# Kernel tuning notes

Measured on AMD Instinct MI355X. Metric: run time of the kernel, lower is better.

The kernel has to match this reference:

```python
import jax, jax.numpy as jnp
import numpy as np

N = 100000
E = 1000000
F_NODE = 64
F_EDGE = 32
H = 128
C_NODE = 12
C_EDGE = 4


def _glorot(key, shape):
    fan_in, fan_out = shape[0], shape[1]
    s = (6.0 / (fan_in + fan_out)) ** 0.5
    return jax.random.uniform(key, shape, jnp.float32, -s, s)


def setup_inputs() -> dict:
    key = jax.random.key(0)
    ks = jax.random.split(key, 16)
    x = jax.random.normal(ks[0], (N, F_NODE), jnp.float32)
    edge_index = jax.random.randint(ks[1], (2, E), 0, N, jnp.int32)
    edge_attr = jax.random.normal(ks[2], (E, F_EDGE), jnp.float32)
    return {
        "x": x,
        "edge_index": edge_index,
        "edge_attr": edge_attr,
        "We": _glorot(ks[3], (F_NODE, H)), "be": jnp.zeros((H,), jnp.float32),
        "Wc1": _glorot(ks[4], (H, H)), "bc1": jnp.zeros((H,), jnp.float32),
        "Wc2": _glorot(ks[5], (H, H)), "bc2": jnp.zeros((H,), jnp.float32),
        "Wn1": _glorot(ks[6], (H, H // 2)), "bn1": jnp.zeros((H // 2,), jnp.float32),
        "Wn2": _glorot(ks[7], (H // 2, C_NODE)), "bn2": jnp.zeros((C_NODE,), jnp.float32),
        "Wedge1": _glorot(ks[8], (2 * H + F_EDGE, H)), "bedge1": jnp.zeros((H,), jnp.float32),
        "Wedge2": _glorot(ks[9], (H, C_EDGE)), "bedge2": jnp.zeros((C_EDGE,), jnp.float32),
    }


def _gcn_conv(x, W, b, src, tgt, n):
    # PyG GCNConv: add self-loops, symmetric deg normalization, scatter-add.
    xw = x @ W  # [N, H]
    loop = jnp.arange(n, dtype=src.dtype)
    s = jnp.concatenate([src, loop])
    t = jnp.concatenate([tgt, loop])
    deg = jax.ops.segment_sum(jnp.ones_like(t, jnp.float32), t, num_segments=n)
    dinv = jnp.where(deg > 0, jax.lax.rsqrt(jnp.maximum(deg, 1.0)), 0.0)
    norm = dinv[s] * dinv[t]  # [E+N]
    msg = xw[s] * norm[:, None]
    return jax.ops.segment_sum(msg, t, num_segments=n) + b


def reference(x, edge_index, edge_attr, We, be, Wc1, bc1, Wc2, bc2,
              Wn1, bn1, Wn2, bn2, Wedge1, bedge1, Wedge2, bedge2):
    n = x.shape[0]
    row, col = edge_index[0], edge_index[1]
    h = jax.nn.relu(x @ We + be)          # node_embed Linear+ReLU
    h = jax.nn.relu(h)                     # extra F.relu in forward
    h = jax.nn.relu(_gcn_conv(h, Wc1, bc1, row, col, n))
    h = jax.nn.relu(_gcn_conv(h, Wc2, bc2, row, col, n))
    node_logits = jax.nn.relu(h @ Wn1 + bn1) @ Wn2 + bn2
    e = jnp.concatenate([h[row], h[col], edge_attr], axis=-1)  # [E, 2H+Fe]
    edge_logits = jax.nn.relu(e @ Wedge1 + bedge1) @ Wedge2 + bedge2
    return (node_logits, edge_logits)
```

## Files before the change

kernel.cpp:

```cpp
#include <hip/hip_runtime.h>

#define N_NODES 100000
#define N_EDGES 1000000
#define NB_SCAN 391
#define EDGE_OUT_BASE 1200000

typedef __attribute__((ext_vector_type(8))) short short8;
typedef __attribute__((ext_vector_type(4))) unsigned short us4;
typedef __attribute__((ext_vector_type(4))) float f32x4;

__device__ __forceinline__ float bf2f(unsigned short u) {
    unsigned int x = ((unsigned int)u) << 16;
    return __builtin_bit_cast(float, x);
}
__device__ __forceinline__ float lo_bf(unsigned int u) {
    return __builtin_bit_cast(float, u << 16);
}
__device__ __forceinline__ float hi_bf(unsigned int u) {
    return __builtin_bit_cast(float, u & 0xffff0000u);
}
__device__ __forceinline__ unsigned short f2bf(float f) {
    unsigned int x = __builtin_bit_cast(unsigned int, f);
    return (unsigned short)((x + 0x7fffu + ((x >> 16) & 1u)) >> 16);
}

__global__ __launch_bounds__(256) void k_detect(const unsigned short* __restrict__ xr,
                                                int* __restrict__ flag) {
    __shared__ int s[256];
    int t = threadIdx.x;
    int cnt = 0;
    for (int i = t; i < 8192; i += 256) {
        int e = (xr[i] >> 7) & 0xFF;
        if (e >= 148) cnt++;
    }
    s[t] = cnt;
    __syncthreads();
    for (int off = 128; off > 0; off >>= 1) {
        if (t < off) s[t] += s[t + off];
        __syncthreads();
    }
    if (t == 0) *flag = (s[0] > 100) ? 1 : 0;
}

struct WPack { const void* p[14]; };
#define W_TOTAL 87888
__global__ __launch_bounds__(256) void k_convw(WPack wp, const int* __restrict__ flag,
                                               unsigned short* __restrict__ dst) {
    const int starts[15] = {0, 8192, 8320, 24704, 24832, 41216, 41344, 49536,
                            49600, 50368, 50380, 87244, 87372, 87884, 87888};
    bool f32 = (*flag != 0);
    int i = blockIdx.x * 256 + threadIdx.x;
    if (i >= W_TOTAL) return;
    int s = 0;
#pragma unroll
    for (int k = 1; k < 14; k++) s += (i >= starts[k]) ? 1 : 0;
    int j = i - starts[s];
    dst[i] = f32 ? f2bf(((const float*)wp.p[s])[j]) : ((const unsigned short*)wp.p[s])[j];
}
#define OW_We 0
#define OW_be 8192
#define OW_Wc1 8320
#define OW_bc1 24704
#define OW_Wc2 24832
#define OW_bc2 41216
#define OW_Wn1 41344
#define OW_bn1 49536
#define OW_Wn2 49600
#define OW_bn2 50368
#define OW_We1 50380
#define OW_be1 87244
#define OW_We2 87372
#define OW_be2 87884

__global__ __launch_bounds__(256) void k_hist(const int* __restrict__ ecol, int* __restrict__ deg) {
    int e = blockIdx.x * 256 + threadIdx.x;
    if (e < N_EDGES) atomicAdd(&deg[ecol[e]], 1);
}

__global__ __launch_bounds__(256) void k_scanA(const int* __restrict__ deg, int* __restrict__ bsum) {
    __shared__ int s[256];
    int i = blockIdx.x * 256 + threadIdx.x;
    s[threadIdx.x] = (i < N_NODES) ? deg[i] : 0;
    __syncthreads();
    for (int off = 128; off > 0; off >>= 1) {
        if (threadIdx.x < off) s[threadIdx.x] += s[threadIdx.x + off];
        __syncthreads();
    }
    if (threadIdx.x == 0) bsum[blockIdx.x] = s[0];
}

__global__ __launch_bounds__(512) void k_scanB(int* __restrict__ bsum) {
    __shared__ int s[512];
    int t = threadIdx.x;
    int v = (t < NB_SCAN) ? bsum[t] : 0;
    s[t] = v;
    __syncthreads();
    for (int off = 1; off < 512; off <<= 1) {
        int x = (t >= off) ? s[t - off] : 0;
        __syncthreads();
        s[t] += x;
        __syncthreads();
    }
    if (t < NB_SCAN) bsum[t] = s[t] - v;
}

__global__ __launch_bounds__(256) void k_scanC(const int* __restrict__ deg, const int* __restrict__ bsum,
                                               int* __restrict__ row_off, int* __restrict__ cursor,
                                               float* __restrict__ dinv) {
    __shared__ int s[256];
    int i = blockIdx.x * 256 + threadIdx.x;
    int t = threadIdx.x;
    int v = (i < N_NODES) ? deg[i] : 0;
    s[t] = v;
    __syncthreads();
    for (int off = 1; off < 256; off <<= 1) {
        int x = (t >= off) ? s[t - off] : 0;
        __syncthreads();
        s[t] += x;
        __syncthreads();
    }
    int excl = s[t] - v + bsum[blockIdx.x];
    if (i < N_NODES) {
        row_off[i] = excl;
        cursor[i] = excl;
        dinv[i] = rsqrtf((float)(v + 1));
    }
    if (i == N_NODES - 1) row_off[N_NODES] = excl + v;
}

__global__ __launch_bounds__(256) void k_fill(const int* __restrict__ erow, const int* __restrict__ ecol,
                                              int* __restrict__ cursor, int* __restrict__ csr) {
    int e = blockIdx.x * 256 + threadIdx.x;
    if (e < N_EDGES) {
        int pos = atomicAdd(&cursor[ecol[e]], 1);
        csr[pos] = erow[e];
    }
}

template <int K, int O, bool RELU, bool BIAS, bool SCALE>
__global__ __launch_bounds__(256) void gemm_rows(const void* __restrict__ A, int M,
                                                 const unsigned short* __restrict__ W, int o_real,
                                                 const unsigned short* __restrict__ bias,
                                                 void* __restrict__ Out, int out_pitch,
                                                 const float* __restrict__ rowscale,
                                                 const int* aflag, const int* oflag) {
    constexpr int KP = K + 8;
    constexpr int KS = K / 32;
    constexpr int OT = O / 16;
    __shared__ short wt[O * KP];
    __shared__ float bias_s[O];
    int tid = threadIdx.x;
    for (int idx = tid; idx < K * O; idx += 256) {
        int k = idx / O, o = idx % O;
        short w = 0;
        if (o < o_real) w = (short)W[(size_t)k * o_real + o];
        wt[o * KP + k] = w;
    }
    if (BIAS) {
        for (int o = tid; o < O; o += 256) bias_s[o] = (o < o_real) ? bf2f(bias[o]) : 0.f;
    }
    __syncthreads();

    bool af32 = aflag && (*aflag != 0);
    bool of32 = oflag && (*oflag != 0);

    int wid = tid >> 6, lane = tid & 63;
    int rbase = (blockIdx.x * 4 + wid) * 32;
    if (rbase >= M) return;
    int lq = lane >> 4, lr = lane & 15;

    short8 a[2][KS];
#pragma unroll
    for (int rg = 0; rg < 2; rg++) {
        int row = rbase + rg * 16 + lr;
        if (row >= M) row = M - 1;
        if (af32) {
            const float* ap = (const float*)A + (size_t)row * K + lq * 8;
#pragma unroll
            for (int ks = 0; ks < KS; ks++) {
                f32x4 u0 = *(const f32x4*)(ap + ks * 32);
                f32x4 u1 = *(const f32x4*)(ap + ks * 32 + 4);
                short8 v;
                v[0] = (short)f2bf(u0[0]); v[1] = (short)f2bf(u0[1]);
                v[2] = (short)f2bf(u0[2]); v[3] = (short)f2bf(u0[3]);
                v[4] = (short)f2bf(u1[0]); v[5] = (short)f2bf(u1[1]);
                v[6] = (short)f2bf(u1[2]); v[7] = (short)f2bf(u1[3]);
                a[rg][ks] = v;
            }
        } else {
            const unsigned short* ap = (const unsigned short*)A + (size_t)row * K + lq * 8;
#pragma unroll
            for (int ks = 0; ks < KS; ks++) a[rg][ks] = *(const short8*)(ap + ks * 32);
        }
    }

    f32x4 acc[2][OT];
#pragma unroll
    for (int rg = 0; rg < 2; rg++)
#pragma unroll
        for (int j = 0; j < OT; j++) {
            acc[rg][j][0] = 0.f; acc[rg][j][1] = 0.f; acc[rg][j][2] = 0.f; acc[rg][j][3] = 0.f;
        }

#pragma unroll
    for (int j = 0; j < OT; j++) {
        short8 b[KS];
#pragma unroll
        for (int ks = 0; ks < KS; ks++)
            b[ks] = *(const short8*)(&wt[(lr + 16 * j) * KP + ks * 32 + lq * 8]);
#pragma unroll
        for (int rg = 0; rg < 2; rg++)
#pragma unroll
            for (int ks = 0; ks < KS; ks++)
                acc[rg][j] = __builtin_amdgcn_mfma_f32_16x16x32_bf16(a[rg][ks], b[ks], acc[rg][j], 0, 0, 0);
    }

#pragma unroll
    for (int rg = 0; rg < 2; rg++)
#pragma unroll
        for (int j = 0; j < OT; j++)
#pragma unroll
            for (int r = 0; r < 4; r++) {
                int row = rbase + rg * 16 + lq * 4 + r;
                int col = lr + 16 * j;
                if (row < M && col < o_real) {
                    float v = acc[rg][j][r];
                    if (BIAS) v += bias_s[col];
                    if (RELU) v = fmaxf(v, 0.f);
                    if (SCALE) v *= rowscale[row];
                    size_t oi = (size_t)row * out_pitch + col;
                    if (of32) ((float*)Out)[oi] = v;
                    else ((unsigned short*)Out)[oi] = f2bf(v);
                }
            }
}

__global__ __launch_bounds__(256) void node_head(const unsigned short* __restrict__ A, int M,
                                                 const unsigned short* __restrict__ wbuf,
                                                 void* __restrict__ Out, const int* oflag) {
    __shared__ short wt1[64 * 136];
    __shared__ short zb[128 * 72];
    __shared__ short wt2[16 * 72];
    __shared__ float b1[64];
    __shared__ float b2[16];
    int tid = threadIdx.x;
    const unsigned short* Wn1 = wbuf + OW_Wn1;
    const unsigned short* Wn2 = wbuf + OW_Wn2;
    for (int idx = tid; idx < 64 * 128; idx += 256) {
        int k = idx >> 6, o = idx & 63;
        wt1[o * 136 + k] = (short)Wn1[idx];
    }
    for (int idx = tid; idx < 16 * 64; idx += 256) {
        int o = idx & 15, k = idx >> 4;
        wt2[o * 72 + k] = (o < 12) ? (short)Wn2[k * 12 + o] : 0;
    }
    if (tid < 64) b1[tid] = bf2f(wbuf[OW_bn1 + tid]);
    if (tid < 16) b2[tid] = (tid < 12) ? bf2f(wbuf[OW_bn2 + tid]) : 0.f;
    __syncthreads();

    bool of32 = oflag && (*oflag != 0);
    int wid = tid >> 6, lane = tid & 63;
    int lq = lane >> 4, lr = lane & 15;
    int rbase = blockIdx.x * 128 + wid * 32;

    short8 a[2][4];
#pragma unroll
    for (int rg = 0; rg < 2; rg++) {
        int row = rbase + rg * 16 + lr;
        if (row >= M) row = M - 1;
        const unsigned short* ap = A + (size_t)row * 128 + lq * 8;
#pragma unroll
        for (int ks = 0; ks < 4; ks++) a[rg][ks] = *(const short8*)(ap + ks * 32);
    }

    {
        f32x4 acc[2][4];
#pragma unroll
        for (int rg = 0; rg < 2; rg++)
#pragma unroll
            for (int j = 0; j < 4; j++) {
                acc[rg][j][0] = 0.f; acc[rg][j][1] = 0.f; acc[rg][j][2] = 0.f; acc[rg][j][3] = 0.f;
            }
#pragma unroll
        for (int j = 0; j < 4; j++) {
            short8 b[4];
#pragma unroll
            for (int ks = 0; ks < 4; ks++)
                b[ks] = *(const short8*)(&wt1[(lr + 16 * j) * 136 + ks * 32 + lq * 8]);
#pragma unroll
            for (int rg = 0; rg < 2; rg++)
#pragma unroll
                for (int ks = 0; ks < 4; ks++)
                    acc[rg][j] = __builtin_amdgcn_mfma_f32_16x16x32_bf16(a[rg][ks], b[ks], acc[rg][j], 0, 0, 0);
        }
#pragma unroll
        for (int rg = 0; rg < 2; rg++)
#pragma unroll
            for (int j = 0; j < 4; j++)
#pragma unroll
                for (int r = 0; r < 4; r++) {
                    int rl = wid * 32 + rg * 16 + lq * 4 + r;
                    int col = lr + 16 * j;
                    zb[rl * 72 + col] = (short)f2bf(fmaxf(acc[rg][j][r] + b1[col], 0.f));
                }
    }
    __syncthreads();

    {
        short8 a2[2][2];
#pragma unroll
        for (int rg = 0; rg < 2; rg++) {
            int rl = wid * 32 + rg * 16 + lr;
#pragma unroll
            for (int ks = 0; ks < 2; ks++)
                a2[rg][ks] = *(const short8*)(&zb[rl * 72 + ks * 32 + lq * 8]);
        }
        short8 b[2];
#pragma unroll
        for (int ks = 0; ks < 2; ks++)
            b[ks] = *(const short8*)(&wt2[lr * 72 + ks * 32 + lq * 8]);
        f32x4 acc[2];
#pragma unroll
        for (int rg = 0; rg < 2; rg++) {
            acc[rg][0] = 0.f; acc[rg][1] = 0.f; acc[rg][2] = 0.f; acc[rg][3] = 0.f;
#pragma unroll
            for (int ks = 0; ks < 2; ks++)
                acc[rg] = __builtin_amdgcn_mfma_f32_16x16x32_bf16(a2[rg][ks], b[ks], acc[rg], 0, 0, 0);
        }
#pragma unroll
        for (int rg = 0; rg < 2; rg++)
#pragma unroll
            for (int r = 0; r < 4; r++) {
                int row = rbase + rg * 16 + lq * 4 + r;
                int col = lr;
                if (row < M && col < 12) {
                    float v = acc[rg][r] + b2[col];
                    size_t oi = (size_t)row * 12 + col;
                    if (of32) ((float*)Out)[oi] = v;
                    else ((unsigned short*)Out)[oi] = f2bf(v);
                }
            }
    }
}

__global__ __launch_bounds__(256) void gemm_pq(const unsigned short* __restrict__ A, int M,
                                               const unsigned short* __restrict__ W1,
                                               const unsigned short* __restrict__ W2,
                                               unsigned short* __restrict__ Pout,
                                               unsigned short* __restrict__ Qout) {
    __shared__ short wt[128 * 136];
    int tid = threadIdx.x;
    int wid = tid >> 6, lane = tid & 63;
    int rbase = (blockIdx.x * 4 + wid) * 32;
    int lq = lane >> 4, lr = lane & 15;

    short8 a[2][4];
#pragma unroll
    for (int rg = 0; rg < 2; rg++) {
        int row = rbase + rg * 16 + lr;
        if (row >= M) row = M - 1;
        const unsigned short* ap = A + (size_t)row * 128 + lq * 8;
#pragma unroll
        for (int ks = 0; ks < 4; ks++) a[rg][ks] = *(const short8*)(ap + ks * 32);
    }

    int pc0 = (lr >> 2) * 32 + (lr & 3);

    for (int idx = tid; idx < 128 * 128; idx += 256) {
        int k = idx >> 7, o = idx & 127;
        wt[o * 136 + k] = (short)W1[idx];
    }
    __syncthreads();
    {
        f32x4 acc[2][8];
#pragma unroll
        for (int rg = 0; rg < 2; rg++)
#pragma unroll
            for (int j = 0; j < 8; j++) {
                acc[rg][j][0] = 0.f; acc[rg][j][1] = 0.f; acc[rg][j][2] = 0.f; acc[rg][j][3] = 0.f;
            }
#pragma unroll
        for (int j = 0; j < 8; j++) {
            short8 b[4];
#pragma unroll
            for (int ks = 0; ks < 4; ks++)
                b[ks] = *(const short8*)(&wt[(lr + 16 * j) * 136 + ks * 32 + lq * 8]);
#pragma unroll
            for (int rg = 0; rg < 2; rg++)
#pragma unroll
                for (int ks = 0; ks < 4; ks++)
                    acc[rg][j] = __builtin_amdgcn_mfma_f32_16x16x32_bf16(a[rg][ks], b[ks], acc[rg][j], 0, 0, 0);
        }
#pragma unroll
        for (int rg = 0; rg < 2; rg++)
#pragma unroll
            for (int j = 0; j < 8; j++)
#pragma unroll
                for (int r = 0; r < 4; r++) {
                    int row = rbase + rg * 16 + lq * 4 + r;
                    if (row < M) Pout[(size_t)row * 128 + pc0 + j * 4] = f2bf(acc[rg][j][r]);
                }
    }
    __syncthreads();

    for (int idx = tid; idx < 128 * 128; idx += 256) {
        int k = idx >> 7, o = idx & 127;
        wt[o * 136 + k] = (short)W2[idx];
    }
    __syncthreads();
    {
        f32x4 acc[2][8];
#pragma unroll
        for (int rg = 0; rg < 2; rg++)
#pragma unroll
            for (int j = 0; j < 8; j++) {
                acc[rg][j][0] = 0.f; acc[rg][j][1] = 0.f; acc[rg][j][2] = 0.f; acc[rg][j][3] = 0.f;
            }
#pragma unroll
        for (int j = 0; j < 8; j++) {
            short8 b[4];
#pragma unroll
            for (int ks = 0; ks < 4; ks++)
                b[ks] = *(const short8*)(&wt[(lr + 16 * j) * 136 + ks * 32 + lq * 8]);
#pragma unroll
            for (int rg = 0; rg < 2; rg++)
#pragma unroll
                for (int ks = 0; ks < 4; ks++)
                    acc[rg][j] = __builtin_amdgcn_mfma_f32_16x16x32_bf16(a[rg][ks], b[ks], acc[rg][j], 0, 0, 0);
        }
#pragma unroll
        for (int rg = 0; rg < 2; rg++)
#pragma unroll
            for (int j = 0; j < 8; j++)
#pragma unroll
                for (int r = 0; r < 4; r++) {
                    int row = rbase + rg * 16 + lq * 4 + r;
                    if (row < M) Qout[(size_t)row * 128 + pc0 + j * 4] = f2bf(acc[rg][j][r]);
                }
    }
}

__global__ __launch_bounds__(256) void conv_kernel(const unsigned short* __restrict__ xw_s,
                                                   const int* __restrict__ csr_src,
                                                   const int* __restrict__ row_off,
                                                   const float* __restrict__ dinv,
                                                   const unsigned short* __restrict__ bias,
                                                   unsigned short* __restrict__ out) {
    int wid = threadIdx.x >> 6, lane = threadIdx.x & 63;
    int base = (blockIdx.x * 4 + wid) * 2;
    int t0 = base, t1 = base + 1;
    int beg0 = row_off[t0], end0 = row_off[t0 + 1];
    int beg1 = row_off[t1], end1 = row_off[t1 + 1];
    float dt0 = dinv[t0], dt1 = dinv[t1];
    unsigned int v0 = *(const unsigned int*)(xw_s + (size_t)t0 * 128 + lane * 2);
    unsigned int v1 = *(const unsigned int*)(xw_s + (size_t)t1 * 128 + lane * 2);
    unsigned int bv = *(const unsigned int*)(bias + lane * 2);
    float a00 = lo_bf(v0), a01 = hi_bf(v0);
    float a10 = lo_bf(v1), a11 = hi_bf(v1);
    int i0 = beg0, i1 = beg1;
    while (i0 + 4 <= end0 && i1 + 4 <= end1) {
        int s00 = csr_src[i0], s01 = csr_src[i0 + 1], s02 = csr_src[i0 + 2], s03 = csr_src[i0 + 3];
        int s10 = csr_src[i1], s11 = csr_src[i1 + 1], s12 = csr_src[i1 + 2], s13 = csr_src[i1 + 3];
        unsigned int u00 = *(const unsigned int*)(xw_s + (size_t)s00 * 128 + lane * 2);
        unsigned int u01 = *(const unsigned int*)(xw_s + (size_t)s01 * 128 + lane * 2);
        unsigned int u02 = *(const unsigned int*)(xw_s + (size_t)s02 * 128 + lane * 2);
        unsigned int u03 = *(const unsigned int*)(xw_s + (size_t)s03 * 128 + lane * 2);
        unsigned int u10 = *(const unsigned int*)(xw_s + (size_t)s10 * 128 + lane * 2);
        unsigned int u11 = *(const unsigned int*)(xw_s + (size_t)s11 * 128 + lane * 2);
        unsigned int u12 = *(const unsigned int*)(xw_s + (size_t)s12 * 128 + lane * 2);
        unsigned int u13 = *(const unsigned int*)(xw_s + (size_t)s13 * 128 + lane * 2);
        a00 += lo_bf(u00) + lo_bf(u01) + lo_bf(u02) + lo_bf(u03);
        a01 += hi_bf(u00) + hi_bf(u01) + hi_bf(u02) + hi_bf(u03);
        a10 += lo_bf(u10) + lo_bf(u11) + lo_bf(u12) + lo_bf(u13);
        a11 += hi_bf(u10) + hi_bf(u11) + hi_bf(u12) + hi_bf(u13);
        i0 += 4; i1 += 4;
    }
    for (; i0 + 4 <= end0; i0 += 4) {
        int s0 = csr_src[i0], s1 = csr_src[i0 + 1], s2 = csr_src[i0 + 2], s3 = csr_src[i0 + 3];
        unsigned int u0 = *(const unsigned int*)(xw_s + (size_t)s0 * 128 + lane * 2);
        unsigned int u1 = *(const unsigned int*)(xw_s + (size_t)s1 * 128 + lane * 2);
        unsigned int u2 = *(const unsigned int*)(xw_s + (size_t)s2 * 128 + lane * 2);
        unsigned int u3 = *(const unsigned int*)(xw_s + (size_t)s3 * 128 + lane * 2);
        a00 += lo_bf(u0) + lo_bf(u1) + lo_bf(u2) + lo_bf(u3);
        a01 += hi_bf(u0) + hi_bf(u1) + hi_bf(u2) + hi_bf(u3);
    }
    for (; i1 + 4 <= end1; i1 += 4) {
        int s0 = csr_src[i1], s1 = csr_src[i1 + 1], s2 = csr_src[i1 + 2], s3 = csr_src[i1 + 3];
        unsigned int u0 = *(const unsigned int*)(xw_s + (size_t)s0 * 128 + lane * 2);
        unsigned int u1 = *(const unsigned int*)(xw_s + (size_t)s1 * 128 + lane * 2);
        unsigned int u2 = *(const unsigned int*)(xw_s + (size_t)s2 * 128 + lane * 2);
        unsigned int u3 = *(const unsigned int*)(xw_s + (size_t)s3 * 128 + lane * 2);
        a10 += lo_bf(u0) + lo_bf(u1) + lo_bf(u2) + lo_bf(u3);
        a11 += hi_bf(u0) + hi_bf(u1) + hi_bf(u2) + hi_bf(u3);
    }
    for (; i0 < end0; i0++) {
        int s = csr_src[i0];
        unsigned int u = *(const unsigned int*)(xw_s + (size_t)s * 128 + lane * 2);
        a00 += lo_bf(u); a01 += hi_bf(u);
    }
    for (; i1 < end1; i1++) {
        int s = csr_src[i1];
        unsigned int u = *(const unsigned int*)(xw_s + (size_t)s * 128 + lane * 2);
        a10 += lo_bf(u); a11 += hi_bf(u);
    }
    a00 = fmaxf(fmaf(a00, dt0, lo_bf(bv)), 0.f);
    a01 = fmaxf(fmaf(a01, dt0, hi_bf(bv)), 0.f);
    a10 = fmaxf(fmaf(a10, dt1, lo_bf(bv)), 0.f);
    a11 = fmaxf(fmaf(a11, dt1, hi_bf(bv)), 0.f);
    unsigned int o0 = (unsigned int)f2bf(a00) | ((unsigned int)f2bf(a01) << 16);
    unsigned int o1 = (unsigned int)f2bf(a10) | ((unsigned int)f2bf(a11) << 16);
    *(unsigned int*)(out + (size_t)t0 * 128 + lane * 2) = o0;
    *(unsigned int*)(out + (size_t)t1 * 128 + lane * 2) = o1;
}

__device__ __forceinline__ void epi_chunk(f32x4& ov, const f32x4& acc_lo, const f32x4& acc_hi,
                                          short8 pv, short8 qv,
                                          const float* __restrict__ b1s,
                                          const float* __restrict__ w2s, int pb) {
#pragma unroll
    for (int jj = 0; jj < 2; jj++) {
        const f32x4& ac = jj ? acc_hi : acc_lo;
#pragma unroll
        for (int r = 0; r < 4; r++) {
            int idx = jj * 4 + r;
            float t = ac[r] + bf2f((unsigned short)pv[idx]) + bf2f((unsigned short)qv[idx]) + b1s[pb + idx];
            t = fmaxf(t, 0.f);
            f32x4 w2v = *(const f32x4*)(&w2s[(pb + idx) * 4]);
            ov[0] = fmaf(t, w2v[0], ov[0]);
            ov[1] = fmaf(t, w2v[1], ov[1]);
            ov[2] = fmaf(t, w2v[2], ov[2]);
            ov[3] = fmaf(t, w2v[3], ov[3]);
        }
    }
}

__global__ __launch_bounds__(256) void edge_head(const void* __restrict__ ea,
                                                 const int* __restrict__ erow, const int* __restrict__ ecol,
                                                 const unsigned short* __restrict__ P,
                                                 const unsigned short* __restrict__ Q,
                                                 const unsigned short* __restrict__ wbuf,
                                                 void* __restrict__ out, const int* dtflag) {
    __shared__ short wct[128 * 40];
    __shared__ float w2s[128 * 4];
    __shared__ float b1s[128];
    int tid = threadIdx.x;
    const unsigned short* Wc3 = wbuf + OW_We1 + 256 * 128;
    for (int idx = tid; idx < 32 * 128; idx += 256) {
        int k = idx >> 7, o = idx & 127;
        wct[o * 40 + k] = (short)Wc3[idx];
    }
    for (int idx = tid; idx < 512; idx += 256) {
        int p = idx >> 2, o = idx & 3;
        int ch = 16 * ((p & 31) >> 2) + 4 * (p >> 5) + (p & 3);
        w2s[idx] = bf2f(wbuf[OW_We2 + ch * 4 + o]);
    }
    if (tid < 128) {
        int p = tid;
        int ch = 16 * ((p & 31) >> 2) + 4 * (p >> 5) + (p & 3);
        b1s[p] = bf2f(wbuf[OW_be1 + ch]);
    }
    __syncthreads();

    bool f32io = (*dtflag != 0);
    int wid = tid >> 6, lane = tid & 63;
    int lq = lane >> 4, lr = lane & 15;
    int tbase = (blockIdx.x * 4 + wid) * 2;
    int e0a = tbase * 16, e0b = e0a + 16;

    int gea = e0a + lr, geb = e0b + lr;
    bool va = gea < N_EDGES, vb = geb < N_EDGES;
    int geca = va ? gea : (N_EDGES - 1);
    int gecb = vb ? geb : (N_EDGES - 1);

    int rna = erow[geca], cna = ecol[geca];
    int rnb = erow[gecb], cnb = ecol[gecb];

    auto load_efrag = [&](int ge) -> short8 {
        short8 v;
        if (f32io) {
            const float* eap = (const float*)ea + (size_t)ge * 32 + lq * 8;
            f32x4 u0 = __builtin_nontemporal_load((const f32x4*)eap);
            f32x4 u1 = __builtin_nontemporal_load((const f32x4*)(eap + 4));
            v[0] = (short)f2bf(u0[0]); v[1] = (short)f2bf(u0[1]);
            v[2] = (short)f2bf(u0[2]); v[3] = (short)f2bf(u0[3]);
            v[4] = (short)f2bf(u1[0]); v[5] = (short)f2bf(u1[1]);
            v[6] = (short)f2bf(u1[2]); v[7] = (short)f2bf(u1[3]);
        } else {
            v = __builtin_nontemporal_load((const short8*)((const unsigned short*)ea + (size_t)ge * 32 + lq * 8));
        }
        return v;
    };
    short8 efA = load_efrag(geca);
    short8 efB = load_efrag(gecb);

    const unsigned short* PpA = P + (size_t)rna * 128 + lq * 32;
    const unsigned short* QpA = Q + (size_t)cna * 128 + lq * 32;
    const unsigned short* PpB = P + (size_t)rnb * 128 + lq * 32;
    const unsigned short* QpB = Q + (size_t)cnb * 128 + lq * 32;

    f32x4 zero; zero[0] = 0.f; zero[1] = 0.f; zero[2] = 0.f; zero[3] = 0.f;
    f32x4 ovA = zero, ovB = zero;

    {
        short8 pA0 = *(const short8*)(PpA + 0);
        short8 pA1 = *(const short8*)(PpA + 8);
        short8 qA0 = *(const short8*)(QpA + 0);
        short8 qA1 = *(const short8*)(QpA + 8);
        short8 pB0 = *(const short8*)(PpB + 0);
        short8 pB1 = *(const short8*)(PpB + 8);
        short8 qB0 = *(const short8*)(QpB + 0);
        short8 qB1 = *(const short8*)(QpB + 8);
        short8 wf0 = *(const short8*)(&wct[(0 * 16 + lr) * 40 + lq * 8]);
        short8 wf1 = *(const short8*)(&wct[(1 * 16 + lr) * 40 + lq * 8]);
        short8 wf2 = *(const short8*)(&wct[(2 * 16 + lr) * 40 + lq * 8]);
        short8 wf3 = *(const short8*)(&wct[(3 * 16 + lr) * 40 + lq * 8]);
        f32x4 aA0 = __builtin_amdgcn_mfma_f32_16x16x32_bf16(wf0, efA, zero, 0, 0, 0);
        f32x4 aA1 = __builtin_amdgcn_mfma_f32_16x16x32_bf16(wf1, efA, zero, 0, 0, 0);
        f32x4 aA2 = __builtin_amdgcn_mfma_f32_16x16x32_bf16(wf2, efA, zero, 0, 0, 0);
        f32x4 aA3 = __builtin_amdgcn_mfma_f32_16x16x32_bf16(wf3, efA, zero, 0, 0, 0);
        f32x4 aB0 = __builtin_amdgcn_mfma_f32_16x16x32_bf16(wf0, efB, zero, 0, 0, 0);
        f32x4 aB1 = __builtin_amdgcn_mfma_f32_16x16x32_bf16(wf1, efB, zero, 0, 0, 0);
        f32x4 aB2 = __builtin_amdgcn_mfma_f32_16x16x32_bf16(wf2, efB, zero, 0, 0, 0);
        f32x4 aB3 = __builtin_amdgcn_mfma_f32_16x16x32_bf16(wf3, efB, zero, 0, 0, 0);
        epi_chunk(ovA, aA0, aA1, pA0, qA0, b1s, w2s, lq * 32 + 0);
        epi_chunk(ovA, aA2, aA3, pA1, qA1, b1s, w2s, lq * 32 + 8);
        epi_chunk(ovB, aB0, aB1, pB0, qB0, b1s, w2s, lq * 32 + 0);
        epi_chunk(ovB, aB2, aB3, pB1, qB1, b1s, w2s, lq * 32 + 8);
    }
    {
        short8 pA0 = *(const short8*)(PpA + 16);
        short8 pA1 = *(const short8*)(PpA + 24);
        short8 qA0 = *(const short8*)(QpA + 16);
        short8 qA1 = *(const short8*)(QpA + 24);
        short8 pB0 = *(const short8*)(PpB + 16);
        short8 pB1 = *(const short8*)(PpB + 24);
        short8 qB0 = *(const short8*)(QpB + 16);
        short8 qB1 = *(const short8*)(QpB + 24);
        short8 wf0 = *(const short8*)(&wct[(4 * 16 + lr) * 40 + lq * 8]);
        short8 wf1 = *(const short8*)(&wct[(5 * 16 + lr) * 40 + lq * 8]);
        short8 wf2 = *(const short8*)(&wct[(6 * 16 + lr) * 40 + lq * 8]);
        short8 wf3 = *(const short8*)(&wct[(7 * 16 + lr) * 40 + lq * 8]);
        f32x4 aA0 = __builtin_amdgcn_mfma_f32_16x16x32_bf16(wf0, efA, zero, 0, 0, 0);
        f32x4 aA1 = __builtin_amdgcn_mfma_f32_16x16x32_bf16(wf1, efA, zero, 0, 0, 0);
        f32x4 aA2 = __builtin_amdgcn_mfma_f32_16x16x32_bf16(wf2, efA, zero, 0, 0, 0);
        f32x4 aA3 = __builtin_amdgcn_mfma_f32_16x16x32_bf16(wf3, efA, zero, 0, 0, 0);
        f32x4 aB0 = __builtin_amdgcn_mfma_f32_16x16x32_bf16(wf0, efB, zero, 0, 0, 0);
        f32x4 aB1 = __builtin_amdgcn_mfma_f32_16x16x32_bf16(wf1, efB, zero, 0, 0, 0);
        f32x4 aB2 = __builtin_amdgcn_mfma_f32_16x16x32_bf16(wf2, efB, zero, 0, 0, 0);
        f32x4 aB3 = __builtin_amdgcn_mfma_f32_16x16x32_bf16(wf3, efB, zero, 0, 0, 0);
        epi_chunk(ovA, aA0, aA1, pA0, qA0, b1s, w2s, lq * 32 + 16);
        epi_chunk(ovA, aA2, aA3, pA1, qA1, b1s, w2s, lq * 32 + 24);
        epi_chunk(ovB, aB0, aB1, pB0, qB0, b1s, w2s, lq * 32 + 16);
        epi_chunk(ovB, aB2, aB3, pB1, qB1, b1s, w2s, lq * 32 + 24);
    }

#pragma unroll
    for (int c = 0; c < 4; c++) {
        ovA[c] += __shfl_xor(ovA[c], 16);
        ovA[c] += __shfl_xor(ovA[c], 32);
        ovB[c] += __shfl_xor(ovB[c], 16);
        ovB[c] += __shfl_xor(ovB[c], 32);
    }
    if (lq == 0) {
        float be2_0 = bf2f(wbuf[OW_be2 + 0]), be2_1 = bf2f(wbuf[OW_be2 + 1]);
        float be2_2 = bf2f(wbuf[OW_be2 + 2]), be2_3 = bf2f(wbuf[OW_be2 + 3]);
        if (va) {
            size_t oi = (size_t)EDGE_OUT_BASE + (size_t)gea * 4;
            if (f32io) {
                f32x4 res; res[0] = ovA[0] + be2_0; res[1] = ovA[1] + be2_1;
                res[2] = ovA[2] + be2_2; res[3] = ovA[3] + be2_3;
                __builtin_nontemporal_store(res, (f32x4*)((float*)out + oi));
            } else {
                us4 res; res[0] = f2bf(ovA[0] + be2_0); res[1] = f2bf(ovA[1] + be2_1);
                res[2] = f2bf(ovA[2] + be2_2); res[3] = f2bf(ovA[3] + be2_3);
                __builtin_nontemporal_store(res, (us4*)((unsigned short*)out + oi));
            }
        }
        if (vb) {
            size_t oi = (size_t)EDGE_OUT_BASE + (size_t)geb * 4;
            if (f32io) {
                f32x4 res; res[0] = ovB[0] + be2_0; res[1] = ovB[1] + be2_1;
                res[2] = ovB[2] + be2_2; res[3] = ovB[3] + be2_3;
                __builtin_nontemporal_store(res, (f32x4*)((float*)out + oi));
            } else {
                us4 res; res[0] = f2bf(ovB[0] + be2_0); res[1] = f2bf(ovB[1] + be2_1);
                res[2] = f2bf(ovB[2] + be2_2); res[3] = f2bf(ovB[3] + be2_3);
                __builtin_nontemporal_store(res, (us4*)((unsigned short*)out + oi));
            }
        }
    }
}

extern "C" void kernel_launch(void* const* d_in, const int* in_sizes, int n_in,
                              void* d_out, int out_size, void* d_ws, size_t ws_size,
                              hipStream_t stream) {
    const void* x = d_in[0];
    const int* ei = (const int*)d_in[1];
    const void* ea = d_in[2];
    const int* erow = ei;
    const int* ecol = ei + N_EDGES;

    char* ws = (char*)d_ws;
    size_t off = 0;
    auto alloc = [&](size_t bytes) -> void* {
        void* p = ws + off;
        off += (bytes + 255) & ~(size_t)255;
        return p;
    };
    unsigned short* Abuf = (unsigned short*)alloc((size_t)N_NODES * 128 * 2);
    unsigned short* Bbuf = (unsigned short*)alloc((size_t)N_NODES * 128 * 2);
    int* deg = (int*)alloc((size_t)N_NODES * 4);
    int* row_off = (int*)alloc((size_t)(N_NODES + 1) * 4);
    int* cursor = (int*)alloc((size_t)N_NODES * 4);
    int* csr = (int*)alloc((size_t)N_EDGES * 4);
    int* bsum = (int*)alloc(512 * 4);
    float* dinv = (float*)alloc((size_t)N_NODES * 4);
    unsigned short* wbuf = (unsigned short*)alloc((size_t)W_TOTAL * 2);
    int* dtflag = (int*)alloc(256);

    k_detect<<<1, 256, 0, stream>>>((const unsigned short*)x, dtflag);

    WPack wp;
    for (int i = 0; i < 14; i++) wp.p[i] = d_in[3 + i];
    k_convw<<<(W_TOTAL + 255) / 256, 256, 0, stream>>>(wp, dtflag, wbuf);

    (void)hipMemsetAsync(deg, 0, (size_t)N_NODES * 4, stream);
    k_hist<<<(N_EDGES + 255) / 256, 256, 0, stream>>>(ecol, deg);
    k_scanA<<<NB_SCAN, 256, 0, stream>>>(deg, bsum);
    k_scanB<<<1, 512, 0, stream>>>(bsum);
    k_scanC<<<NB_SCAN, 256, 0, stream>>>(deg, bsum, row_off, cursor, dinv);
    k_fill<<<(N_EDGES + 255) / 256, 256, 0, stream>>>(erow, ecol, cursor, csr);

    int gB = (N_NODES + 127) / 128;
    gemm_rows<64, 128, true, true, false><<<gB, 256, 0, stream>>>(x, N_NODES, wbuf + OW_We, 128, wbuf + OW_be, Abuf, 128, nullptr, dtflag, nullptr);
    gemm_rows<128, 128, false, false, true><<<gB, 256, 0, stream>>>(Abuf, N_NODES, wbuf + OW_Wc1, 128, nullptr, Bbuf, 128, dinv, nullptr, nullptr);
    conv_kernel<<<N_NODES / 8, 256, 0, stream>>>(Bbuf, csr, row_off, dinv, wbuf + OW_bc1, Abuf);
    gemm_rows<128, 128, false, false, true><<<gB, 256, 0, stream>>>(Abuf, N_NODES, wbuf + OW_Wc2, 128, nullptr, Bbuf, 128, dinv, nullptr, nullptr);
    conv_kernel<<<N_NODES / 8, 256, 0, stream>>>(Bbuf, csr, row_off, dinv, wbuf + OW_bc2, Abuf);
    node_head<<<gB, 256, 0, stream>>>(Abuf, N_NODES, wbuf, d_out, dtflag);
    gemm_pq<<<gB, 256, 0, stream>>>(Abuf, N_NODES, wbuf + OW_We1, wbuf + OW_We1 + 128 * 128, Bbuf, Abuf);
    edge_head<<<(N_EDGES + 127) / 128, 256, 0, stream>>>(ea, erow, ecol, Bbuf, Abuf, wbuf, d_out, dtflag);
}
```

Measured before the change: 546.2 us.

## Process edge head in CSR (target-sorted) order for Q-row locality

k_fill now also records each CSR slot's original edge id and target node. The edge head kernel walks edges in target-sorted order, so consecutive lanes share the same Q row and those gathers get better cache reuse. Edge attributes are now gathered by original edge id, and outputs presumably scatter by that id. This costs an extra 8 MB write in k_fill and an 8-byte aux read per edge, and makes the edge_attr loads non-contiguous.

```diff
diff --git a/kernel.cpp b/kernel.cpp
--- a/kernel.cpp
+++ b/kernel.cpp
@@ -129,11 +129,14 @@
 }
 
 __global__ __launch_bounds__(256) void k_fill(const int* __restrict__ erow, const int* __restrict__ ecol,
-                                              int* __restrict__ cursor, int* __restrict__ csr) {
+                                              int* __restrict__ cursor, int* __restrict__ csr,
+                                              int2* __restrict__ aux) {
     int e = blockIdx.x * 256 + threadIdx.x;
     if (e < N_EDGES) {
-        int pos = atomicAdd(&cursor[ecol[e]], 1);
+        int c = ecol[e];
+        int pos = atomicAdd(&cursor[c], 1);
         csr[pos] = erow[e];
+        aux[pos] = make_int2(e, c);
     }
 }
 
@@ -535,7 +538,8 @@
 }
 
 __global__ __launch_bounds__(256) void edge_head(const void* __restrict__ ea,
-                                                 const int* __restrict__ erow, const int* __restrict__ ecol,
+                                                 const int* __restrict__ csr_src,
+                                                 const int2* __restrict__ aux,
                                                  const unsigned short* __restrict__ P,
                                                  const unsigned short* __restrict__ Q,
                                                  const unsigned short* __restrict__ wbuf,
@@ -565,15 +569,17 @@
     int wid = tid >> 6, lane = tid & 63;
     int lq = lane >> 4, lr = lane & 15;
     int tbase = (blockIdx.x * 4 + wid) * 2;
-    int e0a = tbase * 16, e0b = e0a + 16;
-
-    int gea = e0a + lr, geb = e0b + lr;
-    bool va = gea < N_EDGES, vb = geb < N_EDGES;
-    int geca = va ? gea : (N_EDGES - 1);
-    int gecb = vb ? geb : (N_EDGES - 1);
-
-    int rna = erow[geca], cna = ecol[geca];
-    int rnb = erow[gecb], cnb = ecol[gecb];
+    int p0a = tbase * 16, p0b = p0a + 16;
+
+    int posa = p0a + lr, posb = p0b + lr;
+    bool va = posa < N_EDGES, vb = posb < N_EDGES;
+    int pca = va ? posa : (N_EDGES - 1);
+    int pcb = vb ? posb : (N_EDGES - 1);
+
+    int rna = csr_src[pca], rnb = csr_src[pcb];
+    int2 axa = aux[pca], axb = aux[pcb];
+    int gea = axa.x, cna = axa.y;
+    int geb = axb.x, cnb = axb.y;
 
     auto load_efrag = [&](int ge) -> short8 {
         short8 v;
@@ -590,8 +596,8 @@
         }
         return v;
     };
-    short8 efA = load_efrag(geca);
-    short8 efB = load_efrag(gecb);
+    short8 efA = load_efrag(gea);
+    short8 efB = load_efrag(geb);
 
     const unsigned short* PpA = P + (size_t)rna * 128 + lq * 32;
     const unsigned short* QpA = Q + (size_t)cna * 128 + lq * 32;
@@ -713,6 +719,7 @@
     int* row_off = (int*)alloc((size_t)(N_NODES + 1) * 4);
     int* cursor = (int*)alloc((size_t)N_NODES * 4);
     int* csr = (int*)alloc((size_t)N_EDGES * 4);
+    int2* aux = (int2*)alloc((size_t)N_EDGES * 8);
     int* bsum = (int*)alloc(512 * 4);
     float* dinv = (float*)alloc((size_t)N_NODES * 4);
     unsigned short* wbuf = (unsigned short*)alloc((size_t)W_TOTAL * 2);
@@ -729,7 +736,7 @@
     k_scanA<<<NB_SCAN, 256, 0, stream>>>(deg, bsum);
     k_scanB<<<1, 512, 0, stream>>>(bsum);
     k_scanC<<<NB_SCAN, 256, 0, stream>>>(deg, bsum, row_off, cursor, dinv);
-    k_fill<<<(N_EDGES + 255) / 256, 256, 0, stream>>>(erow, ecol, cursor, csr);
+    k_fill<<<(N_EDGES + 255) / 256, 256, 0, stream>>>(erow, ecol, cursor, csr, aux);
 
     int gB = (N_NODES + 127) / 128;
     gemm_rows<64, 128, true, true, false><<<gB, 256, 0, stream>>>(x, N_NODES, wbuf + OW_We, 128, wbuf + OW_be, Abuf, 128, nullptr, dtflag, nullptr);
@@ -739,5 +746,5 @@
     conv_kernel<<<N_NODES / 8, 256, 0, stream>>>(Bbuf, csr, row_off, dinv, wbuf + OW_bc2, Abuf);
     node_head<<<gB, 256, 0, stream>>>(Abuf, N_NODES, wbuf, d_out, dtflag);
     gemm_pq<<<gB, 256, 0, stream>>>(Abuf, N_NODES, wbuf + OW_We1, wbuf + OW_We1 + 128 * 128, Bbuf, Abuf);
-    edge_head<<<(N_EDGES + 127) / 128, 256, 0, stream>>>(ea, erow, ecol, Bbuf, Abuf, wbuf, d_out, dtflag);
-}
+    edge_head<<<(N_EDGES + 127) / 128, 256, 0, stream>>>(ea, csr, aux, Bbuf, Abuf, wbuf, d_out, dtflag);
+}
```

Result: faster. 530.9 us (-2.8%).
